# Optimization experiments

Hardware: AMD Instinct MI355X
Metric: run time of the kernel (lower is better)

## Reference

```python
import jax, jax.numpy as jnp
import numpy as np

N = 50000
E = 800000
R = 5
D = 128
Q = D // 4  # 32


def setup_inputs() -> dict:
    key = jax.random.key(0)
    ks = jax.random.split(key, 24)
    s = 0.05
    inp = {
        'des': jax.random.normal(ks[0], (N, 768), jnp.float32),
        'tweet': jax.random.normal(ks[1], (N, 768), jnp.float32),
        'num_prop': jax.random.normal(ks[2], (N, 6), jnp.float32),
        'cat_prop': jax.random.normal(ks[3], (N, 11), jnp.float32),
        'edge_index': jax.random.randint(ks[4], (2, E), 0, N, dtype=jnp.int32),
        'edge_type': jax.random.randint(ks[5], (E,), 0, R, dtype=jnp.int32),
        'W_des': jax.random.normal(ks[6], (768, Q), jnp.float32) * s,
        'b_des': jnp.zeros((Q,), jnp.float32),
        'W_tw': jax.random.normal(ks[7], (768, Q), jnp.float32) * s,
        'b_tw': jnp.zeros((Q,), jnp.float32),
        'W_np': jax.random.normal(ks[8], (6, Q), jnp.float32) * s,
        'b_np': jnp.zeros((Q,), jnp.float32),
        'W_cp': jax.random.normal(ks[9], (11, Q), jnp.float32) * s,
        'b_cp': jnp.zeros((Q,), jnp.float32),
        'W_in': jax.random.normal(ks[10], (D, D), jnp.float32) * s,
        'b_in': jnp.zeros((D,), jnp.float32),
        'rel_w': jax.random.normal(ks[11], (R, D, D), jnp.float32) * s,
        'root_w': jax.random.normal(ks[12], (D, D), jnp.float32) * s,
        'rgcn_b': jnp.zeros((D,), jnp.float32),
        'W_o1': jax.random.normal(ks[13], (D, D), jnp.float32) * s,
        'b_o1': jnp.zeros((D,), jnp.float32),
        'W_o2': jax.random.normal(ks[14], (D, 2), jnp.float32) * s,
        'b_o2': jnp.zeros((2,), jnp.float32),
    }
    return inp


def _lrelu(v):
    return jax.nn.leaky_relu(v, negative_slope=0.01)


def _rgcn(x, edge_index, edge_type, rel_w, root_w, rgcn_b):
    # PyG RGCNConv with default mean aggregation per relation.
    n = x.shape[0]
    src, dst = edge_index[0], edge_index[1]
    h = jnp.einsum('nd,rde->rne', x, rel_w)          # [R, N, D]
    msg = h[edge_type, src]                          # [E, D] gather per edge
    seg = dst * R + edge_type                        # combined (node, relation) key
    sums = jax.ops.segment_sum(msg, seg, num_segments=n * R).reshape(n, R, -1)
    cnt = jax.ops.segment_sum(jnp.ones(msg.shape[0], jnp.float32), seg,
                              num_segments=n * R).reshape(n, R, 1)
    agg = (sums / jnp.maximum(cnt, 1.0)).sum(axis=1)  # mean per relation, sum over relations
    return agg + x @ root_w + rgcn_b


def reference(des, tweet, num_prop, cat_prop, edge_index, edge_type,
              W_des, b_des, W_tw, b_tw, W_np, b_np, W_cp, b_cp,
              W_in, b_in, rel_w, root_w, rgcn_b, W_o1, b_o1, W_o2, b_o2):
    d = _lrelu(des @ W_des + b_des)
    t = _lrelu(tweet @ W_tw + b_tw)
    n_ = _lrelu(num_prop @ W_np + b_np)
    c = _lrelu(cat_prop @ W_cp + b_cp)
    x = jnp.concatenate([d, t, n_, c], axis=1)       # [N, D]
    x = _lrelu(x @ W_in + b_in)
    for _ in range(4):
        x = _rgcn(x, edge_index, edge_type, rel_w, root_w, rgcn_b)
    x = _lrelu(x @ W_o1 + b_o1)
    return x @ W_o2 + b_o2                            # [N, 2]
```

## Files before the change

### kernel.cpp

```cpp
#include <hip/hip_runtime.h>


#define N_NODES 50000
#define N_EDGES 800000
#define R_REL   5
#define NSEG    (N_NODES * R_REL)
#define SCAN_BS 1024
#define SCAN_NB ((NSEG + SCAN_BS - 1) / SCAN_BS)

typedef __attribute__((ext_vector_type(8))) short bf16x8;
typedef __attribute__((ext_vector_type(4))) float f32x4;

__device__ __forceinline__ float lrelu(float v) { return v > 0.f ? v : 0.01f * v; }

__device__ __forceinline__ unsigned short f2bf_rne(float f) {
    unsigned u = __float_as_uint(f);
    return (unsigned short)((u + 0x7fff + ((u >> 16) & 1)) >> 16);
}

__device__ __forceinline__ void split1(float f, short& h, short& l) {
    unsigned u = __float_as_uint(f);
    unsigned short hh = (unsigned short)(u >> 16);
    h = (short)hh;
    l = (short)f2bf_rne(f - __uint_as_float((unsigned)hh << 16));
}

__device__ __forceinline__ void split8(const float* f, bf16x8& hi, bf16x8& lo) {
#pragma unroll
    for (int i = 0; i < 8; i++) {
        short h, l;
        split1(f[i], h, l);
        hi[i] = h;
        lo[i] = l;
    }
}

__global__ __launch_bounds__(256) void count_kernel(const int* __restrict__ ei,
                                                    const int* __restrict__ et,
                                                    int* __restrict__ cnt) {
    int e = blockIdx.x * 256 + threadIdx.x;
    if (e >= N_EDGES) return;
    atomicAdd(&cnt[ei[N_EDGES + e] * R_REL + et[e]], 1);
}

__global__ __launch_bounds__(SCAN_BS) void scan1(const int* __restrict__ cnt,
                                                 int* __restrict__ rowptr,
                                                 int* __restrict__ blockSums) {
    __shared__ int s[SCAN_BS];
    int t = threadIdx.x;
    int i = blockIdx.x * SCAN_BS + t;
    int v = (i < NSEG) ? cnt[i] : 0;
    s[t] = v;
    __syncthreads();
#pragma unroll
    for (int off = 1; off < SCAN_BS; off <<= 1) {
        int add = (t >= off) ? s[t - off] : 0;
        __syncthreads();
        s[t] += add;
        __syncthreads();
    }
    if (i < NSEG) rowptr[i] = s[t] - v;
    if (t == SCAN_BS - 1) blockSums[blockIdx.x] = s[t];
}

__global__ __launch_bounds__(256) void scan2(int* __restrict__ blockSums) {
    __shared__ int s[256];
    int t = threadIdx.x;
    int v = (t < SCAN_NB) ? blockSums[t] : 0;
    s[t] = v;
    __syncthreads();
#pragma unroll
    for (int off = 1; off < 256; off <<= 1) {
        int add = (t >= off) ? s[t - off] : 0;
        __syncthreads();
        s[t] += add;
        __syncthreads();
    }
    if (t < SCAN_NB) blockSums[t] = s[t] - v;
}

__global__ __launch_bounds__(SCAN_BS) void scan3(int* __restrict__ rowptr,
                                                 const int* __restrict__ blockSums) {
    int i = blockIdx.x * SCAN_BS + threadIdx.x;
    if (i == 0) rowptr[NSEG] = N_EDGES;
    if (i < NSEG) rowptr[i] += blockSums[blockIdx.x];
}

__global__ __launch_bounds__(256) void fill_kernel(const int* __restrict__ ei,
                                                   const int* __restrict__ et,
                                                   const int* __restrict__ rowptr,
                                                   int* __restrict__ cursor,
                                                   int* __restrict__ srcSorted) {
    int e = blockIdx.x * 256 + threadIdx.x;
    if (e >= N_EDGES) return;
    int seg = ei[N_EDGES + e] * R_REL + et[e];
    int pos = atomicAdd(&cursor[seg], 1);
    srcSorted[rowptr[seg] + pos] = ei[e];
}

__global__ __launch_bounds__(256) void build_bswz(const float* __restrict__ W,
                                                  int K, int NC, int NTILES,
                                                  short* __restrict__ out) {
    int tid = blockIdx.x * 256 + threadIdx.x;
    int total = (K / 32) * NTILES * 64;
    if (tid >= total) return;
    int l  = tid & 63;
    int nt = (tid >> 6) % NTILES;
    int c  = tid / (64 * NTILES);
    int n = nt * 16 + (l & 15);
    int k0 = c * 32 + (l >> 4) * 8;
    float f[8];
#pragma unroll
    for (int j = 0; j < 8; j++) f[j] = W[(size_t)(k0 + j) * NC + n];
    bf16x8 hi, lo;
    split8(f, hi, lo);
    size_t base = (size_t)c * (2 * NTILES * 512);
    *(bf16x8*)(out + base + ((size_t)nt * 64 + l) * 8) = hi;
    *(bf16x8*)(out + base + (size_t)NTILES * 512 + ((size_t)nt * 64 + l) * 8) = lo;
}

__global__ __launch_bounds__(256) void rgcn_fused(const float* __restrict__ xf,
                                                  const int* __restrict__ rowptr,
                                                  const int* __restrict__ srcSorted,
                                                  const short* __restrict__ bz,
                                                  const float* __restrict__ rgcn_b,
                                                  float* __restrict__ xn, int M) {
    __shared__ short AhS[2][4][2048];
    __shared__ short AlS[2][4][2048];
    const int t = threadIdx.x;
    const int m0 = blockIdx.x * 64;
    const int w = t >> 6, l = t & 63;
    const int q = l >> 4, ln = l & 15;
    const int mw = w >> 1, nw = w & 1;
    const int rr = w * 16 + (t & 15);
    const int qq = (t >> 4) & 3;
    const int node = m0 + rr;
    const int sidx = w * 512 + l * 8;

    f32x4 acc[2][4];
#pragma unroll
    for (int mt = 0; mt < 2; mt++)
#pragma unroll
        for (int nt = 0; nt < 4; nt++) acc[mt][nt] = (f32x4)0.f;

    auto AGG = [&](int rel, int nb) {
        float ag[4][8];
#pragma unroll
        for (int c = 0; c < 4; c++)
#pragma unroll
            for (int j = 0; j < 8; j++) ag[c][j] = 0.f;
        int beg = 0, end = 0;
        if (node < M) {
            int s = node * R_REL + rel;
            beg = rowptr[s];
            end = rowptr[s + 1];
        }
        int i = beg;
        for (; i + 1 < end; i += 2) {
            int s0 = srcSorted[i];
            int s1 = srcSorted[i + 1];
            const float* p0 = xf + (size_t)s0 * 128 + qq * 8;
            const float* p1 = xf + (size_t)s1 * 128 + qq * 8;
#pragma unroll
            for (int c = 0; c < 4; c++) {
                float4 a0 = *(const float4*)(p0 + c * 32);
                float4 a1 = *(const float4*)(p0 + c * 32 + 4);
                float4 b0 = *(const float4*)(p1 + c * 32);
                float4 b1 = *(const float4*)(p1 + c * 32 + 4);
                ag[c][0] += a0.x + b0.x; ag[c][1] += a0.y + b0.y;
                ag[c][2] += a0.z + b0.z; ag[c][3] += a0.w + b0.w;
                ag[c][4] += a1.x + b1.x; ag[c][5] += a1.y + b1.y;
                ag[c][6] += a1.z + b1.z; ag[c][7] += a1.w + b1.w;
            }
        }
        if (i < end) {
            int s0 = srcSorted[i];
            const float* p0 = xf + (size_t)s0 * 128 + qq * 8;
#pragma unroll
            for (int c = 0; c < 4; c++) {
                float4 a0 = *(const float4*)(p0 + c * 32);
                float4 a1 = *(const float4*)(p0 + c * 32 + 4);
                ag[c][0] += a0.x; ag[c][1] += a0.y; ag[c][2] += a0.z; ag[c][3] += a0.w;
                ag[c][4] += a1.x; ag[c][5] += a1.y; ag[c][6] += a1.z; ag[c][7] += a1.w;
            }
        }
        int cnum = end - beg;
        float inv = cnum > 0 ? 1.f / (float)cnum : 0.f;
#pragma unroll
        for (int c = 0; c < 4; c++) {
            bf16x8 hv, lv;
#pragma unroll
            for (int j = 0; j < 8; j++) {
                short hh, ll;
                split1(ag[c][j] * inv, hh, ll);
                hv[j] = hh; lv[j] = ll;
            }
            *(bf16x8*)&AhS[nb][c][sidx] = hv;
            *(bf16x8*)&AlS[nb][c][sidx] = lv;
        }
    };

    auto ROOT = [&](int nb) {
        int gr = node < M ? node : M - 1;
        const float* p0 = xf + (size_t)gr * 128 + qq * 8;
#pragma unroll
        for (int c = 0; c < 4; c++) {
            float f[8];
            *(float4*)&f[0] = *(const float4*)(p0 + c * 32);
            *(float4*)&f[4] = *(const float4*)(p0 + c * 32 + 4);
            bf16x8 hv, lv;
            split8(f, hv, lv);
            *(bf16x8*)&AhS[nb][c][sidx] = hv;
            *(bf16x8*)&AlS[nb][c][sidx] = lv;
        }
    };

    auto GEMMP = [&](const short* bzr, int nb) {
        bf16x8 BH[2][4], BL[2][4];
#pragma unroll
        for (int nt = 0; nt < 4; nt++) {
            const short* bp = bzr + (nw * 4 + nt) * 512 + l * 8;
            BH[0][nt] = *(const bf16x8*)(bp);
            BL[0][nt] = *(const bf16x8*)(bp + 4096);
        }
#pragma unroll
        for (int c = 0; c < 4; c++) {
            if (c < 3) {
#pragma unroll
                for (int nt = 0; nt < 4; nt++) {
                    const short* bp = bzr + (c + 1) * 8192 + (nw * 4 + nt) * 512 + l * 8;
                    BH[(c + 1) & 1][nt] = *(const bf16x8*)(bp);
                    BL[(c + 1) & 1][nt] = *(const bf16x8*)(bp + 4096);
                }
            }
            bf16x8 ah[2], al[2];
#pragma unroll
            for (int mt = 0; mt < 2; mt++) {
                ah[mt] = *(const bf16x8*)&AhS[nb][c][(mw * 2 + mt) * 512 + l * 8];
                al[mt] = *(const bf16x8*)&AlS[nb][c][(mw * 2 + mt) * 512 + l * 8];
            }
#pragma unroll
            for (int nt = 0; nt < 4; nt++) {
                bf16x8 bh = BH[c & 1][nt];
                bf16x8 bl2 = BL[c & 1][nt];
#pragma unroll
                for (int mt = 0; mt < 2; mt++) {
                    acc[mt][nt] = __builtin_amdgcn_mfma_f32_16x16x32_bf16(ah[mt], bh, acc[mt][nt], 0, 0, 0);
                    acc[mt][nt] = __builtin_amdgcn_mfma_f32_16x16x32_bf16(ah[mt], bl2, acc[mt][nt], 0, 0, 0);
                    acc[mt][nt] = __builtin_amdgcn_mfma_f32_16x16x32_bf16(al[mt], bh, acc[mt][nt], 0, 0, 0);
                }
            }
        }
    };

    AGG(0, 0);
    __syncthreads();
#pragma unroll
    for (int r = 0; r < 5; r++) {
        GEMMP(bz + (size_t)r * 32768, r & 1);
        if (r < 4) AGG(r + 1, (r + 1) & 1);
        else ROOT((r + 1) & 1);
        __syncthreads();
    }
    GEMMP(bz + (size_t)5 * 32768, 1);

#pragma unroll
    for (int nt = 0; nt < 4; nt++) {
        int col = (nw * 4 + nt) * 16 + ln;
        float bv = rgcn_b[col];
#pragma unroll
        for (int mt = 0; mt < 2; mt++) {
            f32x4 v = acc[mt][nt];
#pragma unroll
            for (int i = 0; i < 4; i++) {
                int m = m0 + (mw * 2 + mt) * 16 + q * 4 + i;
                if (m < M) xn[(size_t)m * 128 + col] = v[i] + bv;
            }
        }
    }
}

template <int NT, bool ACT>
__global__ __launch_bounds__(256) void mfma_gemm(const float* __restrict__ A, int K,
                                                 const short* __restrict__ Bswz,
                                                 const float* __restrict__ bias,
                                                 float* __restrict__ C, int M,
                                                 int colofs) {
    constexpr int NH = NT / 2;
    __shared__ short Ahi[2048], Alo[2048];
    __shared__ short Bs[NT * 1024];
    const int t = threadIdx.x;
    const int m0 = blockIdx.x * 64;
    const int w = t >> 6, l = t & 63;
    const int q = l >> 4, ln = l & 15;
    const int mw = w >> 1, nw = w & 1;

    f32x4 acc[2][NH];
#pragma unroll
    for (int mt = 0; mt < 2; mt++)
#pragma unroll
        for (int nt = 0; nt < NH; nt++) acc[mt][nt] = (f32x4)0.f;

    const int nchunks = K / 32;
    const int r = t >> 2, qq = t & 3;
    const int aidx = (r >> 4) * 512 + qq * 128 + (r & 15) * 8;
    int gr = m0 + r; if (gr >= M) gr = M - 1;

    for (int c = 0; c < nchunks; c++) {
        __syncthreads();
        {
            const float* ap = A + (size_t)gr * K + c * 32 + qq * 8;
            float f[8];
            *(float4*)&f[0] = ((const float4*)ap)[0];
            *(float4*)&f[4] = ((const float4*)ap)[1];
            bf16x8 h0, l0;
            split8(f, h0, l0);
            *(bf16x8*)&Ahi[aidx] = h0;
            *(bf16x8*)&Alo[aidx] = l0;
        }
        {
            const short* gb = Bswz + (size_t)c * (NT * 1024);
#pragma unroll
            for (int i = 0; i < NH; i++) {
                int idx = i * 256 + t;
                *(bf16x8*)&Bs[idx * 8] = *(const bf16x8*)(gb + (size_t)idx * 8);
            }
        }
        __syncthreads();

        bf16x8 a_hi[2], a_lo[2];
#pragma unroll
        for (int mt = 0; mt < 2; mt++) {
            a_hi[mt] = *(const bf16x8*)&Ahi[(mw * 2 + mt) * 512 + l * 8];
            a_lo[mt] = *(const bf16x8*)&Alo[(mw * 2 + mt) * 512 + l * 8];
        }
#pragma unroll
        for (int nt = 0; nt < NH; nt++) {
            int ng = nw * NH + nt;
            bf16x8 bh = *(const bf16x8*)&Bs[(ng * 64 + l) * 8];
            bf16x8 bl = *(const bf16x8*)&Bs[NT * 512 + (ng * 64 + l) * 8];
#pragma unroll
            for (int mt = 0; mt < 2; mt++) {
                acc[mt][nt] = __builtin_amdgcn_mfma_f32_16x16x32_bf16(a_hi[mt], bh, acc[mt][nt], 0, 0, 0);
                acc[mt][nt] = __builtin_amdgcn_mfma_f32_16x16x32_bf16(a_hi[mt], bl, acc[mt][nt], 0, 0, 0);
                acc[mt][nt] = __builtin_amdgcn_mfma_f32_16x16x32_bf16(a_lo[mt], bh, acc[mt][nt], 0, 0, 0);
            }
        }
    }

#pragma unroll
    for (int nt = 0; nt < NH; nt++) {
        int ng = nw * NH + nt;
        int col = colofs + ng * 16 + ln;
        float bv = bias[ng * 16 + ln];
#pragma unroll
        for (int mt = 0; mt < 2; mt++) {
            f32x4 v = acc[mt][nt];
#pragma unroll
            for (int i = 0; i < 4; i++) {
                int m = m0 + (mw * 2 + mt) * 16 + q * 4 + i;
                if (m < M) {
                    float xv = v[i] + bv;
                    if (ACT) xv = lrelu(xv);
                    C[(size_t)m * 128 + col] = xv;
                }
            }
        }
    }
}

__global__ __launch_bounds__(256) void encode_small(const float* __restrict__ num_prop,
                                                    const float* __restrict__ cat_prop,
                                                    const float* __restrict__ W_np,
                                                    const float* __restrict__ b_np,
                                                    const float* __restrict__ W_cp,
                                                    const float* __restrict__ b_cp,
                                                    float* __restrict__ x) {
    int t = blockIdx.x * 256 + threadIdx.x;
    int node = t >> 6;
    int jj = t & 63;
    if (node >= N_NODES) return;
    if (jj < 32) {
        float acc = b_np[jj];
        const float* row = num_prop + (size_t)node * 6;
#pragma unroll
        for (int k = 0; k < 6; k++) acc = fmaf(row[k], W_np[k * 32 + jj], acc);
        x[(size_t)node * 128 + 64 + jj] = lrelu(acc);
    } else {
        int j = jj - 32;
        float acc = b_cp[j];
        const float* row = cat_prop + (size_t)node * 11;
#pragma unroll
        for (int k = 0; k < 11; k++) acc = fmaf(row[k], W_cp[k * 32 + j], acc);
        x[(size_t)node * 128 + 96 + j] = lrelu(acc);
    }
}

__global__ __launch_bounds__(256) void out_proj(const float* __restrict__ X,
                                                const float* __restrict__ W,
                                                const float* __restrict__ b,
                                                float* __restrict__ out, int M) {
    int n = blockIdx.x * 256 + threadIdx.x;
    if (n >= M) return;
    float a0 = b[0], a1 = b[1];
    const float4* xr = (const float4*)(X + (size_t)n * 128);
#pragma unroll
    for (int k4 = 0; k4 < 32; k4++) {
        float4 v = xr[k4];
        a0 = fmaf(v.x, W[(k4 * 4 + 0) * 2 + 0], a0);
        a1 = fmaf(v.x, W[(k4 * 4 + 0) * 2 + 1], a1);
        a0 = fmaf(v.y, W[(k4 * 4 + 1) * 2 + 0], a0);
        a1 = fmaf(v.y, W[(k4 * 4 + 1) * 2 + 1], a1);
        a0 = fmaf(v.z, W[(k4 * 4 + 2) * 2 + 0], a0);
        a1 = fmaf(v.z, W[(k4 * 4 + 2) * 2 + 1], a1);
        a0 = fmaf(v.w, W[(k4 * 4 + 3) * 2 + 0], a0);
        a1 = fmaf(v.w, W[(k4 * 4 + 3) * 2 + 1], a1);
    }
    out[(size_t)n * 2 + 0] = a0;
    out[(size_t)n * 2 + 1] = a1;
}

static inline size_t align64(size_t x) { return (x + 63) & ~(size_t)63; }

extern "C" void kernel_launch(void* const* d_in, const int* in_sizes, int n_in,
                              void* d_out, int out_size, void* d_ws, size_t ws_size,
                              hipStream_t stream) {
    const float* des      = (const float*)d_in[0];
    const float* tweet    = (const float*)d_in[1];
    const float* num_prop = (const float*)d_in[2];
    const float* cat_prop = (const float*)d_in[3];
    const int*   edge_index = (const int*)d_in[4];
    const int*   edge_type  = (const int*)d_in[5];
    const float* W_des = (const float*)d_in[6];  const float* b_des = (const float*)d_in[7];
    const float* W_tw  = (const float*)d_in[8];  const float* b_tw  = (const float*)d_in[9];
    const float* W_np  = (const float*)d_in[10]; const float* b_np  = (const float*)d_in[11];
    const float* W_cp  = (const float*)d_in[12]; const float* b_cp  = (const float*)d_in[13];
    const float* W_in  = (const float*)d_in[14]; const float* b_in  = (const float*)d_in[15];
    const float* rel_w = (const float*)d_in[16]; const float* root_w = (const float*)d_in[17];
    const float* rgcn_b = (const float*)d_in[18];
    const float* W_o1  = (const float*)d_in[19]; const float* b_o1  = (const float*)d_in[20];
    const float* W_o2  = (const float*)d_in[21]; const float* b_o2  = (const float*)d_in[22];
    float* out = (float*)d_out;

    char* p = (char*)d_ws;
    float* xA  = (float*)p;            p += (size_t)N_NODES * 128 * 4;
    float* xB  = (float*)p;            p += (size_t)N_NODES * 128 * 4;
    int* cnt       = (int*)p;          p += (size_t)NSEG * 4;
    int* rowptr    = (int*)p;          p += (size_t)(NSEG + 1) * 4;
    int* cursor    = (int*)p;          p += (size_t)NSEG * 4;
    int* srcSorted = (int*)p;          p += (size_t)N_EDGES * 4;
    int* blockSums = (int*)p;          p += (size_t)256 * 4;
    p = (char*)align64((size_t)p);
    short* bz_cat = (short*)p;         p += (size_t)6 * 32768 * 2;
    short* bz_in  = (short*)p;         p += (size_t)32768 * 2;
    short* bz_o1  = (short*)p;         p += (size_t)32768 * 2;
    short* bz_des = (short*)p;         p += (size_t)24 * 2048 * 2;
    short* bz_tw  = (short*)p;         p += (size_t)24 * 2048 * 2;

    for (int r = 0; r < R_REL; r++)
        build_bswz<<<8, 256, 0, stream>>>(rel_w + (size_t)r * 128 * 128, 128, 128, 8,
                                          bz_cat + (size_t)r * 32768);
    build_bswz<<<8, 256, 0, stream>>>(root_w, 128, 128, 8, bz_cat + (size_t)5 * 32768);
    build_bswz<<<8, 256, 0, stream>>>(W_in, 128, 128, 8, bz_in);
    build_bswz<<<8, 256, 0, stream>>>(W_o1, 128, 128, 8, bz_o1);
    build_bswz<<<12, 256, 0, stream>>>(W_des, 768, 32, 2, bz_des);
    build_bswz<<<12, 256, 0, stream>>>(W_tw, 768, 32, 2, bz_tw);

    hipMemsetAsync(cnt, 0, (size_t)NSEG * sizeof(int), stream);
    hipMemsetAsync(cursor, 0, (size_t)NSEG * sizeof(int), stream);
    count_kernel<<<(N_EDGES + 255) / 256, 256, 0, stream>>>(edge_index, edge_type, cnt);
    scan1<<<SCAN_NB, SCAN_BS, 0, stream>>>(cnt, rowptr, blockSums);
    scan2<<<1, 256, 0, stream>>>(blockSums);
    scan3<<<SCAN_NB, SCAN_BS, 0, stream>>>(rowptr, blockSums);
    fill_kernel<<<(N_EDGES + 255) / 256, 256, 0, stream>>>(
        edge_index, edge_type, rowptr, cursor, srcSorted);

    const int gm = (N_NODES + 63) / 64;

    encode_small<<<(N_NODES * 64 + 255) / 256, 256, 0, stream>>>(
        num_prop, cat_prop, W_np, b_np, W_cp, b_cp, xA);
    mfma_gemm<2, true><<<gm, 256, 0, stream>>>(des, 768, bz_des, b_des, xA, N_NODES, 0);
    mfma_gemm<2, true><<<gm, 256, 0, stream>>>(tweet, 768, bz_tw, b_tw, xA, N_NODES, 32);

    mfma_gemm<8, true><<<gm, 256, 0, stream>>>(xA, 128, bz_in, b_in, xB, N_NODES, 0);

    float* cur = xB; float* nxt = xA;
    for (int lyr = 0; lyr < 4; lyr++) {
        rgcn_fused<<<gm, 256, 0, stream>>>(cur, rowptr, srcSorted, bz_cat, rgcn_b, nxt, N_NODES);
        float* tmp = cur; cur = nxt; nxt = tmp;
    }

    mfma_gemm<8, true><<<gm, 256, 0, stream>>>(cur, 128, bz_o1, b_o1, nxt, N_NODES, 0);
    out_proj<<<(N_NODES + 255) / 256, 256, 0, stream>>>(nxt, W_o2, b_o2, out, N_NODES);
}
```

Baseline: 1.100 ms.

## Single-buffer RGCN A tiles, roll relation loop, and raise occupancy bound

Replaces the double-buffered shared-memory A tiles with a single buffer, halving LDS use. The relation loop is no longer unrolled and each stage now runs gather, sync, then GEMM, which adds a second barrier per relation. Launch bounds now request 5 blocks per SM to cap register use. The aim is more resident waves to hide the latency of the irregular edge gathers. The cost is losing the overlap between aggregation and GEMM, plus possible register spills.

```diff
diff --git a/kernel.cpp b/kernel.cpp
--- a/kernel.cpp
+++ b/kernel.cpp
@@ -119,14 +119,14 @@
     *(bf16x8*)(out + base + (size_t)NTILES * 512 + ((size_t)nt * 64 + l) * 8) = lo;
 }
 
-__global__ __launch_bounds__(256) void rgcn_fused(const float* __restrict__ xf,
-                                                  const int* __restrict__ rowptr,
-                                                  const int* __restrict__ srcSorted,
-                                                  const short* __restrict__ bz,
-                                                  const float* __restrict__ rgcn_b,
-                                                  float* __restrict__ xn, int M) {
-    __shared__ short AhS[2][4][2048];
-    __shared__ short AlS[2][4][2048];
+__global__ __launch_bounds__(256, 5) void rgcn_fused(const float* __restrict__ xf,
+                                                     const int* __restrict__ rowptr,
+                                                     const int* __restrict__ srcSorted,
+                                                     const short* __restrict__ bz,
+                                                     const float* __restrict__ rgcn_b,
+                                                     float* __restrict__ xn, int M) {
+    __shared__ short AhS[4][2048];
+    __shared__ short AlS[4][2048];
     const int t = threadIdx.x;
     const int m0 = blockIdx.x * 64;
     const int w = t >> 6, l = t & 63;
@@ -143,7 +143,7 @@
 #pragma unroll
         for (int nt = 0; nt < 4; nt++) acc[mt][nt] = (f32x4)0.f;
 
-    auto AGG = [&](int rel, int nb) {
+    auto AGG = [&](int rel) {
         float ag[4][8];
 #pragma unroll
         for (int c = 0; c < 4; c++)
@@ -195,12 +195,12 @@
                 split1(ag[c][j] * inv, hh, ll);
                 hv[j] = hh; lv[j] = ll;
             }
-            *(bf16x8*)&AhS[nb][c][sidx] = hv;
-            *(bf16x8*)&AlS[nb][c][sidx] = lv;
+            *(bf16x8*)&AhS[c][sidx] = hv;
+            *(bf16x8*)&AlS[c][sidx] = lv;
         }
     };
 
-    auto ROOT = [&](int nb) {
+    auto ROOT = [&]() {
         int gr = node < M ? node : M - 1;
         const float* p0 = xf + (size_t)gr * 128 + qq * 8;
 #pragma unroll
@@ -210,12 +210,12 @@
             *(float4*)&f[4] = *(const float4*)(p0 + c * 32 + 4);
             bf16x8 hv, lv;
             split8(f, hv, lv);
-            *(bf16x8*)&AhS[nb][c][sidx] = hv;
-            *(bf16x8*)&AlS[nb][c][sidx] = lv;
+            *(bf16x8*)&AhS[c][sidx] = hv;
+            *(bf16x8*)&AlS[c][sidx] = lv;
         }
     };
 
-    auto GEMMP = [&](const short* bzr, int nb) {
+    auto GEMMP = [&](const short* bzr) {
         bf16x8 BH[2][4], BL[2][4];
 #pragma unroll
         for (int nt = 0; nt < 4; nt++) {
@@ -236,8 +236,8 @@
             bf16x8 ah[2], al[2];
 #pragma unroll
             for (int mt = 0; mt < 2; mt++) {
-                ah[mt] = *(const bf16x8*)&AhS[nb][c][(mw * 2 + mt) * 512 + l * 8];
-                al[mt] = *(const bf16x8*)&AlS[nb][c][(mw * 2 + mt) * 512 + l * 8];
+                ah[mt] = *(const bf16x8*)&AhS[c][(mw * 2 + mt) * 512 + l * 8];
+                al[mt] = *(const bf16x8*)&AlS[c][(mw * 2 + mt) * 512 + l * 8];
             }
 #pragma unroll
             for (int nt = 0; nt < 4; nt++) {
@@ -253,16 +253,13 @@
         }
     };
 
-    AGG(0, 0);
-    __syncthreads();
-#pragma unroll
-    for (int r = 0; r < 5; r++) {
-        GEMMP(bz + (size_t)r * 32768, r & 1);
-        if (r < 4) AGG(r + 1, (r + 1) & 1);
-        else ROOT((r + 1) & 1);
-        __syncthreads();
-    }
-    GEMMP(bz + (size_t)5 * 32768, 1);
+#pragma unroll 1
+    for (int r = 0; r < 6; r++) {
+        if (r > 0) __syncthreads();
+        if (r < 5) AGG(r); else ROOT();
+        __syncthreads();
+        GEMMP(bz + (size_t)r * 32768);
+    }
 
 #pragma unroll
     for (int nt = 0; nt < 4; nt++) {
```

Measured after the change: 1.042 ms. 1.06x faster.
